# Performance work log

Hardware: AMD Instinct MI355X
Metric: run time of the kernel (lower is better)

## Reference

```python
import jax, jax.numpy as jnp
import numpy as np

N_NODES = 50000
N_EDGES = 800000
NEG_SLOPE = 0.2  # GATConv default
BN_EPS = 1e-5


def _seg_softmax(logits, seg, n):
    # per-target-node softmax over incoming edges (PyG softmax w/ +1e-16)
    m = jax.ops.segment_max(logits, seg, num_segments=n)
    m = jnp.where(jnp.isfinite(m), m, 0.0)
    e = jnp.exp(logits - m[seg])
    s = jax.ops.segment_sum(e, seg, num_segments=n)
    return e / (s[seg] + 1e-16)


def _gat_conv(x, src, dst, W, a_src, a_dst, b, concat):
    # x: [N, Fin]; W: [Fin, H*C]; a_src/a_dst: [H, C]
    n = x.shape[0]
    H, C = a_src.shape
    h = (x @ W).reshape(n, H, C)
    al_s = jnp.einsum('nhc,hc->nh', h, a_src)
    al_d = jnp.einsum('nhc,hc->nh', h, a_dst)
    logits = jax.nn.leaky_relu(al_s[src] + al_d[dst], NEG_SLOPE)  # [E, H]
    alpha = _seg_softmax(logits, dst, n)                           # [E, H]
    out = jax.ops.segment_sum(h[src] * alpha[:, :, None], dst, num_segments=n)
    out = out.reshape(n, H * C) if concat else out.mean(axis=1)
    return out + b


def _bn(x, g, b):
    mu = jnp.mean(x, axis=0)
    var = jnp.mean((x - mu) ** 2, axis=0)
    return (x - mu) * jax.lax.rsqrt(var + BN_EPS) * g + b


def _gat_params(key, fin, heads, ch, scale=0.1):
    k1, k2, k3 = jax.random.split(key, 3)
    W = jax.random.normal(k1, (fin, heads * ch), jnp.float32) * scale
    a_s = jax.random.normal(k2, (heads, ch), jnp.float32) * scale
    a_d = jax.random.normal(k3, (heads, ch), jnp.float32) * scale
    return W, a_s, a_d


def setup_inputs() -> dict:
    key = jax.random.key(0)
    ks = jax.random.split(key, 12)
    inp = {}
    inp['x'] = jax.random.normal(ks[0], (N_NODES, 3), jnp.float32)
    inp['edge_index'] = jax.random.randint(ks[1], (2, N_EDGES), 0, N_NODES, jnp.int64 if jax.config.jax_enable_x64 else jnp.int32)
    inp['W11'], inp['as11'], inp['ad11'] = _gat_params(ks[2], 3, 8, 8)
    inp['b11'] = jnp.zeros((64,), jnp.float32)
    inp['W12'], inp['as12'], inp['ad12'] = _gat_params(ks[3], 64, 8, 8)
    inp['b12'] = jnp.zeros((64,), jnp.float32)
    inp['g1'] = jnp.ones((64,), jnp.float32)
    inp['be1'] = jnp.zeros((64,), jnp.float32)
    inp['W21'], inp['as21'], inp['ad21'] = _gat_params(ks[4], 64, 8, 32)
    inp['b21'] = jnp.zeros((256,), jnp.float32)
    inp['W22'], inp['as22'], inp['ad22'] = _gat_params(ks[5], 256, 8, 32)
    inp['b22'] = jnp.zeros((256,), jnp.float32)
    inp['g2'] = jnp.ones((256,), jnp.float32)
    inp['be2'] = jnp.zeros((256,), jnp.float32)
    inp['W31'], inp['as31'], inp['ad31'] = _gat_params(ks[6], 256, 8, 64)
    inp['b31'] = jnp.zeros((512,), jnp.float32)
    inp['W32'], inp['as32'], inp['ad32'] = _gat_params(ks[7], 512, 8, 1)
    inp['b32'] = jnp.zeros((1,), jnp.float32)
    return inp


def reference(x, edge_index,
              W11, as11, ad11, b11, W12, as12, ad12, b12, g1, be1,
              W21, as21, ad21, b21, W22, as22, ad22, b22, g2, be2,
              W31, as31, ad31, b31, W32, as32, ad32, b32):
    n = x.shape[0]
    loops = jnp.arange(n, dtype=edge_index.dtype)
    src = jnp.concatenate([edge_index[0], loops])  # add_self_loops=True
    dst = jnp.concatenate([edge_index[1], loops])
    # GAT(3, 64, 2): conv -> relu -> conv
    h = jax.nn.relu(_gat_conv(x, src, dst, W11, as11, ad11, b11, True))
    h = _gat_conv(h, src, dst, W12, as12, ad12, b12, True)
    h = jax.nn.leaky_relu(_bn(h, g1, be1), 0.1)
    # GAT(64, 256, 2)
    h = jax.nn.relu(_gat_conv(h, src, dst, W21, as21, ad21, b21, True))
    h = _gat_conv(h, src, dst, W22, as22, ad22, b22, True)
    h = jax.nn.leaky_relu(_bn(h, g2, be2), 0.1)
    # GAT(256, 512, 2, 1): conv -> relu -> conv(concat=False)
    h = jax.nn.relu(_gat_conv(h, src, dst, W31, as31, ad31, b31, True))
    h = _gat_conv(h, src, dst, W32, as32, ad32, b32, False)
    return jax.nn.sigmoid(h)
```

## Files before the change

kernel.cpp:

```cpp
#include <hip/hip_runtime.h>
#include <math.h>

typedef short short8 __attribute__((ext_vector_type(8)));
typedef short short4v __attribute__((ext_vector_type(4)));
typedef float f32x4 __attribute__((ext_vector_type(4)));

__device__ __forceinline__ unsigned short f2bf(float v){
  unsigned u = __builtin_bit_cast(unsigned, v);
  u += 0x7FFFu + ((u >> 16) & 1u);
  return (unsigned short)(u >> 16);
}
__device__ __forceinline__ float bf2f(unsigned short b){
  unsigned u = ((unsigned)b) << 16;
  return __builtin_bit_cast(float, u);
}

__global__ void k_deg(const int* __restrict__ dstv, int* __restrict__ deg, int E){
  int e = blockIdx.x*blockDim.x + threadIdx.x;
  if (e < E) atomicAdd(&deg[dstv[e]], 1);
}

__global__ void k_scan(const int* __restrict__ deg, int* __restrict__ off,
                       int* __restrict__ cursor, int N){
  __shared__ int wpre[16];
  __shared__ int s_tot;
  __shared__ int carry;
  int tid = threadIdx.x;
  int lane = tid & 63, wv = tid >> 6;
  if (tid == 0) carry = 0;
  __syncthreads();
  for (int base = 0; base < N; base += 1024){
    int i = base + tid;
    int v = (i < N) ? deg[i] : 0;
    int incl = v;
    #pragma unroll
    for (int d = 1; d < 64; d <<= 1){
      int t = __shfl_up(incl, d, 64);
      if (lane >= d) incl += t;
    }
    if (lane == 63) wpre[wv] = incl;
    __syncthreads();
    if (tid < 16){
      int x = wpre[tid];
      int ix = x;
      #pragma unroll
      for (int d = 1; d < 16; d <<= 1){
        int t = __shfl_up(ix, d, 16);
        if (tid >= d) ix += t;
      }
      wpre[tid] = ix - x;
      if (tid == 15) s_tot = ix;
    }
    __syncthreads();
    int c = carry;
    int excl = c + wpre[wv] + (incl - v);
    if (i < N){ off[i+1] = excl + v; cursor[i] = excl; }
    __syncthreads();
    if (tid == 0) carry = c + s_tot;
    __syncthreads();
  }
  if (tid == 0) off[0] = 0;
}

__global__ void k_fill(const int* __restrict__ srcv, const int* __restrict__ dstv,
                       int* __restrict__ cursor, int* __restrict__ csr, int E){
  int e = blockIdx.x*blockDim.x + threadIdx.x;
  if (e < E){
    int d = dstv[e];
    int p = atomicAdd(&cursor[d], 1);
    csr[p] = srcv[e];
  }
}

__global__ void k_prepAll(const float* __restrict__ W11, const float* __restrict__ W12,
                          const float* __restrict__ W21, const float* __restrict__ W22,
                          const float* __restrict__ W31,
                          unsigned short* __restrict__ bh, unsigned short* __restrict__ bl){
  int i = blockIdx.x*blockDim.x + threadIdx.x;
  if (i >= 221184) return;
  const float* W; int K, kpsh, off, Nn;
  if (i < 4096)       { W=W11; K=3;   kpsh=6; off=0;     Nn=64;  }
  else if (i < 8192)  { W=W12; K=64;  kpsh=6; off=4096;  Nn=64;  }
  else if (i < 24576) { W=W21; K=64;  kpsh=6; off=8192;  Nn=256; }
  else if (i < 90112) { W=W22; K=256; kpsh=8; off=24576; Nn=256; }
  else                { W=W31; K=256; kpsh=8; off=90112; Nn=512; }
  int j = i - off;
  int Kp = 1 << kpsh;
  int n = j >> kpsh, k = j & (Kp-1);
  float v = (k < K) ? W[(size_t)k*Nn + n] : 0.0f;
  unsigned short h = f2bf(v);
  bh[i] = h;
  bl[i] = f2bf(v - bf2f(h));
}

__global__ void k_bn_stats(const unsigned short* __restrict__ x, float* __restrict__ psum,
                           float* __restrict__ psq, int N, int HC){
  int f = threadIdx.x;
  float s = 0.f, q = 0.f;
  for (int r = blockIdx.x; r < N; r += gridDim.x){
    float v = bf2f(x[(size_t)r*HC + f]);
    s += v; q += v*v;
  }
  psum[blockIdx.x*HC + f] = s;
  psq [blockIdx.x*HC + f] = q;
}

__global__ void k_bn_coef(const float* __restrict__ psum, const float* __restrict__ psq,
                          const float* __restrict__ g, const float* __restrict__ b,
                          float* __restrict__ sc, float* __restrict__ sh,
                          float invN, int HC, int nb){
  int f = threadIdx.x + blockIdx.x*blockDim.x;
  if (f >= HC) return;
  float s = 0.f, q = 0.f;
  for (int r = 0; r < nb; ++r){ s += psum[r*HC+f]; q += psq[r*HC+f]; }
  float mu  = s*invN;
  float var = q*invN - mu*mu;
  float rs  = rsqrtf(var + 1e-5f) * g[f];
  sc[f] = rs;
  sh[f] = b[f] - mu*rs;
}

template<int BN, int AFMT>
__global__ __launch_bounds__((BN==64)?256:512)
void gemm_mfma(const void* __restrict__ Av, const unsigned short* __restrict__ Bh,
               const unsigned short* __restrict__ Bl,
               const float* __restrict__ bnsc, const float* __restrict__ bnsh,
               const float* __restrict__ a_s, const float* __restrict__ a_d,
               unsigned short* __restrict__ Pb, float* __restrict__ Ds,
               float* __restrict__ Dd, int M, int K){
  constexpr int WAVES   = (BN==64) ? 4 : 8;
  constexpr int BLOCK   = WAVES*64;
  constexpr int WAVES_N = BN/64;
  constexpr int WAVES_M = WAVES/WAVES_N;
  constexpr int WM      = 64/WAVES_M;
  constexpr int MF      = WM/16;
  constexpr int CH      = (BN==512)?64 : (BN==256)?32 : 8;
  constexpr int TERMS   = (AFMT==2) ? 2 : 3;
  const int Kp = (K + 63) & ~(int)63;

  __shared__ char lds[(TERMS==3)?16384:8192];

  int tid  = threadIdx.x;
  int lane = tid & 63;
  int wid  = tid >> 6;
  int wn = wid % WAVES_N;
  int wm = wid / WAVES_N;
  int n0w = wn*64;
  int wm0 = wm*WM;
  int m0 = blockIdx.x * 64;

  f32x4 acc[MF][4];
  #pragma unroll
  for (int i = 0; i < MF; ++i)
    #pragma unroll
    for (int j = 0; j < 4; ++j)
      acc[i][j] = (f32x4){0.f,0.f,0.f,0.f};

  constexpr int SITER = 512/BLOCK;

  for (int k0 = 0; k0 < Kp; k0 += 64){
    __syncthreads();
    #pragma unroll
    for (int it = 0; it < SITER; ++it){
      int i = it*BLOCK + tid;
      int row = i >> 3, c8 = i & 7;
      int gm = m0 + row;
      int gk = k0 + c8*8;
      int off = row*128 + ((c8 ^ (row&7))<<4);
      if constexpr (AFMT == 2){
        short8 hv = {0,0,0,0,0,0,0,0};
        if (gm < M) hv = *(const short8*)((const unsigned short*)Av + (size_t)gm*K + gk);
        *(short8*)(lds + off) = hv;
      } else if constexpr (AFMT == 1){
        short8 raw = {0,0,0,0,0,0,0,0};
        if (gm < M) raw = *(const short8*)((const unsigned short*)Av + (size_t)gm*K + gk);
        short8 hi, lo;
        #pragma unroll
        for (int j=0;j<8;++j){
          float u = bf2f((unsigned short)raw[j])*bnsc[gk+j] + bnsh[gk+j];
          u = u > 0.f ? u : 0.1f*u;
          if (gm >= M) u = 0.f;
          unsigned short hb = f2bf(u);
          hi[j] = (short)hb;
          lo[j] = (short)f2bf(u - bf2f(hb));
        }
        *(short8*)(lds + off) = hi;
        *(short8*)(lds + 8192 + off) = lo;
      } else {
        const float* A = (const float*)Av;
        float v[8];
        if (gm < M && gk + 8 <= K){
          const float* ap = A + (size_t)gm*K + gk;
          float4 x0 = *(const float4*)ap;
          float4 x1 = *(const float4*)(ap+4);
          v[0]=x0.x; v[1]=x0.y; v[2]=x0.z; v[3]=x0.w;
          v[4]=x1.x; v[5]=x1.y; v[6]=x1.z; v[7]=x1.w;
        } else {
          #pragma unroll
          for (int j=0;j<8;++j){
            int gkj = gk + j;
            v[j] = (gm < M && gkj < K) ? A[(size_t)gm*K + gkj] : 0.0f;
          }
        }
        short8 hi, lo;
        #pragma unroll
        for (int j=0;j<8;++j){
          unsigned short hb = f2bf(v[j]);
          hi[j] = (short)hb;
          lo[j] = (short)f2bf(v[j] - bf2f(hb));
        }
        *(short8*)(lds + off) = hi;
        *(short8*)(lds + 8192 + off) = lo;
      }
    }
    __syncthreads();
    #pragma unroll
    for (int kk = 0; kk < 2; ++kk){
      short8 bhf[4], blf[4];
      #pragma unroll
      for (int nf = 0; nf < 4; ++nf){
        int ncol = n0w + nf*16 + (lane & 15);
        int kidx = k0 + kk*32 + ((lane>>4)<<3);
        size_t bo = (size_t)ncol*Kp + kidx;
        bhf[nf] = *(const short8*)(Bh + bo);
        blf[nf] = *(const short8*)(Bl + bo);
      }
      #pragma unroll
      for (int mt = 0; mt < MF; ++mt){
        int row = wm0 + mt*16 + (lane & 15);
        int c8 = kk*4 + (lane>>4);
        int off = row*128 + ((c8 ^ (row&7))<<4);
        short8 ah = *(const short8*)(lds + off);
        #pragma unroll
        for (int nf = 0; nf < 4; ++nf){
          acc[mt][nf] = __builtin_amdgcn_mfma_f32_16x16x32_bf16(ah, bhf[nf], acc[mt][nf], 0,0,0);
          acc[mt][nf] = __builtin_amdgcn_mfma_f32_16x16x32_bf16(ah, blf[nf], acc[mt][nf], 0,0,0);
        }
        if constexpr (TERMS == 3){
          short8 al = *(const short8*)(lds + 8192 + off);
          #pragma unroll
          for (int nf = 0; nf < 4; ++nf)
            acc[mt][nf] = __builtin_amdgcn_mfma_f32_16x16x32_bf16(al, bhf[nf], acc[mt][nf], 0,0,0);
        }
      }
    }
  }

  float asv[4], adv[4];
  #pragma unroll
  for (int nf=0; nf<4; ++nf){
    int gcol = n0w + nf*16 + (lane&15);
    asv[nf] = a_s[gcol];
    adv[nf] = a_d[gcol];
  }
  #pragma unroll
  for (int mt = 0; mt < MF; ++mt){
    #pragma unroll
    for (int r = 0; r < 4; ++r){
      int gm = m0 + wm0 + mt*16 + ((lane>>4)<<2) + r;
      bool ok = gm < M;
      #pragma unroll
      for (int nf=0;nf<4;++nf){
        if (ok) Pb[(size_t)gm*BN + n0w + nf*16 + (lane&15)] = f2bf(acc[mt][nf][r]);
      }
      if constexpr (CH == 64){
        float ps = acc[mt][0][r]*asv[0] + acc[mt][1][r]*asv[1]
                 + acc[mt][2][r]*asv[2] + acc[mt][3][r]*asv[3];
        float pd = acc[mt][0][r]*adv[0] + acc[mt][1][r]*adv[1]
                 + acc[mt][2][r]*adv[2] + acc[mt][3][r]*adv[3];
        #pragma unroll
        for (int d2=1; d2<16; d2<<=1){ ps += __shfl_xor(ps,d2,64); pd += __shfl_xor(pd,d2,64); }
        if (ok && (lane&15)==0){
          int head = n0w >> 6;
          Ds[(size_t)gm*8 + head] = ps;
          Dd[(size_t)gm*8 + head] = pd;
        }
      } else if constexpr (CH == 32){
        float ps0 = acc[mt][0][r]*asv[0] + acc[mt][1][r]*asv[1];
        float ps1 = acc[mt][2][r]*asv[2] + acc[mt][3][r]*asv[3];
        float pd0 = acc[mt][0][r]*adv[0] + acc[mt][1][r]*adv[1];
        float pd1 = acc[mt][2][r]*adv[2] + acc[mt][3][r]*adv[3];
        #pragma unroll
        for (int d2=1; d2<16; d2<<=1){
          ps0 += __shfl_xor(ps0,d2,64); ps1 += __shfl_xor(ps1,d2,64);
          pd0 += __shfl_xor(pd0,d2,64); pd1 += __shfl_xor(pd1,d2,64);
        }
        if (ok && (lane&15)==0){
          int head = n0w >> 5;
          Ds[(size_t)gm*8 + head]     = ps0;
          Ds[(size_t)gm*8 + head + 1] = ps1;
          Dd[(size_t)gm*8 + head]     = pd0;
          Dd[(size_t)gm*8 + head + 1] = pd1;
        }
      } else {
        #pragma unroll
        for (int nf=0;nf<4;++nf){
          float ps = acc[mt][nf][r]*asv[nf];
          float pd = acc[mt][nf][r]*adv[nf];
          #pragma unroll
          for (int d2=1; d2<8; d2<<=1){ ps += __shfl_xor(ps,d2,64); pd += __shfl_xor(pd,d2,64); }
          if (ok && (lane&7)==0){
            int head = nf*2 + ((lane>>3)&1);
            Ds[(size_t)gm*8 + head] = ps;
            Dd[(size_t)gm*8 + head] = pd;
          }
        }
      }
    }
  }
}

template<int HC, int ACT>
__global__ __launch_bounds__(256)
void k_agg(const unsigned short* __restrict__ Pb, const float* __restrict__ Ds,
           const float* __restrict__ Dd, const int* __restrict__ off,
           const int* __restrict__ csr, const float* __restrict__ bias,
           unsigned short* __restrict__ outb, int N){
  constexpr int R = HC/64;
  constexpr int UF = (R==1) ? 8 : 4;
  __shared__ float salpha[4][512];
  int lane = threadIdx.x & 63;
  int wid  = threadIdx.x >> 6;
  int n = blockIdx.x*4 + wid;
  if (n >= N) return;
  int o0 = off[n], deg = off[n+1]-o0;
  int myh = lane >> 3;

  float aldn[8];
  {
    const float* dn = Dd + (unsigned)n*8u;
    float4 x0 = *(const float4*)dn;
    float4 x1 = *(const float4*)(dn+4);
    aldn[0]=x0.x; aldn[1]=x0.y; aldn[2]=x0.z; aldn[3]=x0.w;
    aldn[4]=x1.x; aldn[5]=x1.y; aldn[6]=x1.z; aldn[7]=x1.w;
  }

  float acc[R];
  #pragma unroll
  for (int j=0;j<R;++j) acc[j]=0.f;

  if (deg < 64){
    int nE = deg + 1;
    int myidx = (lane < deg) ? csr[o0+lane] : n;
    bool active = (lane < nE);
    float v[8];
    {
      const float* dp = Ds + (unsigned)myidx*8u;
      float4 x0 = *(const float4*)dp;
      float4 x1 = *(const float4*)(dp+4);
      float t[8] = {x0.x,x0.y,x0.z,x0.w,x1.x,x1.y,x1.z,x1.w};
      #pragma unroll
      for (int h=0;h<8;++h){
        float u = t[h] + aldn[h];
        u = u > 0.f ? u : 0.2f*u;
        v[h] = active ? u : -1e30f;
      }
    }
    float m[8];
    #pragma unroll
    for (int h=0;h<8;++h) m[h]=v[h];
    #pragma unroll
    for (int d=1; d<64; d<<=1)
      #pragma unroll
      for (int h=0;h<8;++h) m[h] = fmaxf(m[h], __shfl_xor(m[h], d, 64));
    float sv[8], s[8];
    #pragma unroll
    for (int h=0;h<8;++h){ sv[h] = active ? __expf(v[h]-m[h]) : 0.f; s[h]=sv[h]; }
    #pragma unroll
    for (int d=1; d<64; d<<=1)
      #pragma unroll
      for (int h=0;h<8;++h) s[h] += __shfl_xor(s[h], d, 64);
    if (active){
      #pragma unroll
      for (int h=0;h<8;++h) salpha[wid][lane*8+h] = sv[h] / (s[h] + 1e-16f);
    }
    asm volatile("s_waitcnt lgkmcnt(0)" ::: "memory");

    const unsigned short* Pl = Pb + lane*R;
    float accu[UF][R];
    #pragma unroll
    for (int u=0;u<UF;++u)
      #pragma unroll
      for (int j=0;j<R;++j) accu[u][j] = 0.f;

    int e = 0;
    #pragma unroll 1
    for (; e + UF <= nE; e += UF){
      unsigned bse[UF];
      float av[UF];
      #pragma unroll
      for (int u=0;u<UF;++u){
        int sidx = __shfl(myidx, e+u, 64);
        bse[u] = (unsigned)sidx * (unsigned)HC;
        av[u]  = salpha[wid][(e+u)*8 + myh];
      }
      #pragma unroll
      for (int u=0;u<UF;++u){
        if constexpr (R == 1){
          accu[u][0] += av[u] * bf2f(Pl[bse[u]]);
        } else if constexpr (R == 4){
          short4v w = *(const short4v*)(Pl + bse[u]);
          #pragma unroll
          for (int j=0;j<4;++j) accu[u][j] += av[u] * bf2f((unsigned short)w[j]);
        } else {
          short8 w = *(const short8*)(Pl + bse[u]);
          #pragma unroll
          for (int j=0;j<8;++j) accu[u][j] += av[u] * bf2f((unsigned short)w[j]);
        }
      }
    }
    #pragma unroll 1
    for (; e < nE; ++e){
      int sidx = __shfl(myidx, e, 64);
      unsigned bs = (unsigned)sidx * (unsigned)HC;
      float alpha = salpha[wid][e*8 + myh];
      if constexpr (R == 1){
        accu[0][0] += alpha * bf2f(Pl[bs]);
      } else if constexpr (R == 4){
        short4v w = *(const short4v*)(Pl + bs);
        #pragma unroll
        for (int j=0;j<4;++j) accu[0][j] += alpha * bf2f((unsigned short)w[j]);
      } else {
        short8 w = *(const short8*)(Pl + bs);
        #pragma unroll
        for (int j=0;j<8;++j) accu[0][j] += alpha * bf2f((unsigned short)w[j]);
      }
    }
    #pragma unroll
    for (int j=0;j<R;++j){
      float t0 = 0.f;
      #pragma unroll
      for (int u=0;u<UF;++u) t0 += accu[u][j];
      acc[j] = t0;
    }
  } else {
    float m[8];
    #pragma unroll
    for (int h=0;h<8;++h) m[h] = -1e30f;
    for (int e = lane; e <= deg; e += 64){
      int src = (e < deg) ? csr[o0+e] : n;
      const float* ap = Ds + (size_t)src*8;
      #pragma unroll
      for (int h=0;h<8;++h){
        float u = ap[h] + aldn[h];
        u = u > 0.f ? u : 0.2f*u;
        m[h] = fmaxf(m[h], u);
      }
    }
    #pragma unroll
    for (int d=1; d<64; d<<=1)
      #pragma unroll
      for (int h=0;h<8;++h) m[h] = fmaxf(m[h], __shfl_xor(m[h], d, 64));
    float s[8] = {0,0,0,0,0,0,0,0};
    for (int e = lane; e <= deg; e += 64){
      int src = (e < deg) ? csr[o0+e] : n;
      const float* ap = Ds + (size_t)src*8;
      #pragma unroll
      for (int h=0;h<8;++h){
        float u = ap[h] + aldn[h];
        u = u > 0.f ? u : 0.2f*u;
        s[h] += __expf(u - m[h]);
      }
    }
    #pragma unroll
    for (int d=1; d<64; d<<=1)
      #pragma unroll
      for (int h=0;h<8;++h) s[h] += __shfl_xor(s[h], d, 64);
    float mh = m[myh];
    float rsh = 1.0f/(s[myh] + 1e-16f);
    float adh = aldn[myh];
    for (int e = 0; e <= deg; ++e){
      int src = (e < deg) ? csr[o0+e] : n;
      float u = Ds[(size_t)src*8 + myh] + adh;
      u = u > 0.f ? u : 0.2f*u;
      float alpha = __expf(u - mh) * rsh;
      const unsigned short* hp = Pb + (size_t)src*HC + lane*R;
      if constexpr (R == 1){
        acc[0] += alpha * bf2f(hp[0]);
      } else if constexpr (R == 4){
        short4v w = *(const short4v*)hp;
        #pragma unroll
        for (int j=0;j<4;++j) acc[j] += alpha * bf2f((unsigned short)w[j]);
      } else {
        short8 w = *(const short8*)hp;
        #pragma unroll
        for (int j=0;j<8;++j) acc[j] += alpha * bf2f((unsigned short)w[j]);
      }
    }
  }

  #pragma unroll
  for (int j = 0; j < R; ++j){
    int f = lane*R + j;
    float v = acc[j] + bias[f];
    if (ACT == 1) v = fmaxf(v, 0.0f);
    outb[(size_t)n*HC + f] = f2bf(v);
  }
}

__global__ __launch_bounds__(256)
void gemm8(const unsigned short* __restrict__ Qb, const float* __restrict__ W,
           float* __restrict__ h8, int M){
  int lane = threadIdx.x & 63;
  int gw = (blockIdx.x*blockDim.x + threadIdx.x) >> 6;
  int nw = (gridDim.x*blockDim.x) >> 6;
  float w[8][8];
  const float* wp = W + lane*64;
  #pragma unroll
  for (int j=0;j<8;++j){
    float4 a = *(const float4*)(wp + j*8);
    float4 b = *(const float4*)(wp + j*8 + 4);
    w[j][0]=a.x; w[j][1]=a.y; w[j][2]=a.z; w[j][3]=a.w;
    w[j][4]=b.x; w[j][5]=b.y; w[j][6]=b.z; w[j][7]=b.w;
  }
  for (int n = gw; n < M; n += nw){
    short8 v8 = *(const short8*)(Qb + (size_t)n*512 + lane*8);
    float p[8] = {0,0,0,0,0,0,0,0};
    #pragma unroll
    for (int j=0;j<8;++j){
      float x = bf2f((unsigned short)v8[j]);
      #pragma unroll
      for (int o=0;o<8;++o) p[o] += x * w[j][o];
    }
    #pragma unroll
    for (int d=1; d<64; d<<=1)
      #pragma unroll
      for (int o=0;o<8;++o) p[o] += __shfl_xor(p[o], d, 64);
    if (lane == 0){
      float4 y0 = make_float4(p[0],p[1],p[2],p[3]);
      float4 y1 = make_float4(p[4],p[5],p[6],p[7]);
      *(float4*)(h8 + (size_t)n*8)     = y0;
      *(float4*)(h8 + (size_t)n*8 + 4) = y1;
    }
  }
}

__global__ __launch_bounds__(256)
void k_final(const float* __restrict__ h8, const float* __restrict__ a_s,
             const float* __restrict__ a_d, const int* __restrict__ off,
             const int* __restrict__ csr, const float* __restrict__ b32,
             float* __restrict__ outp, int N){
  int lane = threadIdx.x & 63;
  int wv   = threadIdx.x >> 6;
  int n = blockIdx.x*4 + wv;
  if (n >= N) return;
  int o0 = off[n], deg = off[n+1]-o0;
  float asv[8], adv[8];
  #pragma unroll
  for (int h=0;h<8;++h){ asv[h]=a_s[h]; adv[h]=a_d[h]; }
  float aldn[8];
  {
    const float* hp = h8 + (size_t)n*8;
    float4 x0 = *(const float4*)hp;
    float4 x1 = *(const float4*)(hp+4);
    float hn[8] = {x0.x,x0.y,x0.z,x0.w,x1.x,x1.y,x1.z,x1.w};
    #pragma unroll
    for (int h=0;h<8;++h) aldn[h] = hn[h]*adv[h];
  }

  if (deg < 64){
    int nE = deg + 1;
    int src = (lane < deg) ? csr[o0+lane] : n;
    bool act = (lane < nE);
    float hs[8];
    {
      const float* hp = h8 + (size_t)src*8;
      float4 x0 = *(const float4*)hp;
      float4 x1 = *(const float4*)(hp+4);
      hs[0]=x0.x; hs[1]=x0.y; hs[2]=x0.z; hs[3]=x0.w;
      hs[4]=x1.x; hs[5]=x1.y; hs[6]=x1.z; hs[7]=x1.w;
    }
    float v[8];
    #pragma unroll
    for (int h=0;h<8;++h){
      float u = hs[h]*asv[h] + aldn[h];
      u = u > 0.f ? u : 0.2f*u;
      v[h] = act ? u : -1e30f;
    }
    float m[8];
    #pragma unroll
    for (int h=0;h<8;++h) m[h]=v[h];
    #pragma unroll
    for (int d=1; d<64; d<<=1)
      #pragma unroll
      for (int h=0;h<8;++h) m[h] = fmaxf(m[h], __shfl_xor(m[h], d, 64));
    float s[8], t[8];
    #pragma unroll
    for (int h=0;h<8;++h){
      float e = act ? __expf(v[h]-m[h]) : 0.f;
      s[h]=e; t[h]=e*hs[h];
    }
    #pragma unroll
    for (int d=1; d<64; d<<=1)
      #pragma unroll
      for (int h=0;h<8;++h){
        s[h] += __shfl_xor(s[h], d, 64);
        t[h] += __shfl_xor(t[h], d, 64);
      }
    if (lane == 0){
      float o = 0.f;
      #pragma unroll
      for (int h=0;h<8;++h) o += t[h]/(s[h]+1e-16f);
      o = o*0.125f + b32[0];
      outp[n] = 1.0f/(1.0f + __expf(-o));
    }
  } else if (lane == 0){
    float m[8], s[8], agg[8];
    #pragma unroll
    for (int h=0;h<8;++h){ m[h]=-1e30f; s[h]=0.f; agg[h]=0.f; }
    for (int e = 0; e <= deg; ++e){
      int src = (e < deg) ? csr[o0+e] : n;
      #pragma unroll
      for (int h=0;h<8;++h){
        float u = h8[(size_t)src*8+h]*asv[h] + aldn[h];
        u = u > 0.f ? u : 0.2f*u;
        m[h] = fmaxf(m[h], u);
      }
    }
    for (int e = 0; e <= deg; ++e){
      int src = (e < deg) ? csr[o0+e] : n;
      #pragma unroll
      for (int h=0;h<8;++h){
        float u = h8[(size_t)src*8+h]*asv[h] + aldn[h];
        u = u > 0.f ? u : 0.2f*u;
        float ex = __expf(u - m[h]);
        s[h] += ex;
        agg[h] += ex * h8[(size_t)src*8+h];
      }
    }
    float o = 0.f;
    #pragma unroll
    for (int h=0;h<8;++h) o += agg[h]/(s[h]+1e-16f);
    o = o*0.125f + b32[0];
    outp[n] = 1.0f/(1.0f + __expf(-o));
  }
}

extern "C" void kernel_launch(void* const* d_in, const int* in_sizes, int n_in,
                              void* d_out, int out_size, void* d_ws, size_t ws_size,
                              hipStream_t stream){
  int N = in_sizes[0]/3;
  int E = in_sizes[1]/2;
  const float* x    = (const float*)d_in[0];
  const int*   ei   = (const int*)  d_in[1];
  const float* W11  = (const float*)d_in[2];
  const float* as11 = (const float*)d_in[3];
  const float* ad11 = (const float*)d_in[4];
  const float* b11  = (const float*)d_in[5];
  const float* W12  = (const float*)d_in[6];
  const float* as12 = (const float*)d_in[7];
  const float* ad12 = (const float*)d_in[8];
  const float* b12  = (const float*)d_in[9];
  const float* g1   = (const float*)d_in[10];
  const float* be1  = (const float*)d_in[11];
  const float* W21  = (const float*)d_in[12];
  const float* as21 = (const float*)d_in[13];
  const float* ad21 = (const float*)d_in[14];
  const float* b21  = (const float*)d_in[15];
  const float* W22  = (const float*)d_in[16];
  const float* as22 = (const float*)d_in[17];
  const float* ad22 = (const float*)d_in[18];
  const float* b22  = (const float*)d_in[19];
  const float* g2   = (const float*)d_in[20];
  const float* be2  = (const float*)d_in[21];
  const float* W31  = (const float*)d_in[22];
  const float* as31 = (const float*)d_in[23];
  const float* ad31 = (const float*)d_in[24];
  const float* b31  = (const float*)d_in[25];
  const float* W32  = (const float*)d_in[26];
  const float* as32 = (const float*)d_in[27];
  const float* ad32 = (const float*)d_in[28];
  const float* b32  = (const float*)d_in[29];

  char* ws = (char*)d_ws;
  size_t o = 0;
  auto alloc = [&](size_t bytes)->char*{
    char* p = ws + o;
    o = (o + bytes + 255) & ~(size_t)255;
    return p;
  };
  int*   deg    = (int*)  alloc((size_t)N*4);
  int*   off    = (int*)  alloc((size_t)(N+1)*4);
  int*   cursor = (int*)  alloc((size_t)N*4);
  int*   csr    = (int*)  alloc((size_t)E*4);
  unsigned short* bh = (unsigned short*)alloc(221184*2);
  unsigned short* bl = (unsigned short*)alloc(221184*2);
  float* h8     = (float*)alloc((size_t)N*8*4);
  float* psum   = (float*)alloc(128*256*4);
  float* psq    = (float*)alloc(128*256*4);
  float* bnsc   = (float*)alloc(1024);
  float* bnsh   = (float*)alloc(1024);
  unsigned short* Pb = (unsigned short*)alloc((size_t)N*512*2);
  unsigned short* Qb = (unsigned short*)alloc((size_t)N*512*2);
  float* Dsb    = (float*)alloc((size_t)N*8*4);
  float* Ddb    = (float*)alloc((size_t)N*8*4);
  (void)ws_size;

  const int BT11=0, BT12=4096, BT21=8192, BT22=24576, BT31=90112;

  hipMemsetAsync(deg, 0, (size_t)N*4, stream);
  int eb = (E+255)/256;
  k_deg <<<eb, 256, 0, stream>>>(ei+E, deg, E);
  k_prepAll<<<(221184+255)/256, 256, 0, stream>>>(W11, W12, W21, W22, W31, bh, bl);
  k_scan<<<1, 1024, 0, stream>>>(deg, off, cursor, N);
  k_fill<<<eb, 256, 0, stream>>>(ei, ei+E, cursor, csr, E);

  int mb = (N+63)/64;
  int nb4 = (N+3)/4;
  float invN = 1.0f/(float)N;

  gemm_mfma<64,0><<<mb, 256, 0, stream>>>(x, bh+BT11, bl+BT11, nullptr, nullptr,
                                          as11, ad11, Pb, Dsb, Ddb, N, 3);
  k_agg<64,1><<<nb4, 256, 0, stream>>>(Pb, Dsb, Ddb, off, csr, b11, Qb, N);

  gemm_mfma<64,2><<<mb, 256, 0, stream>>>(Qb, bh+BT12, bl+BT12, nullptr, nullptr,
                                          as12, ad12, Pb, Dsb, Ddb, N, 64);
  k_agg<64,0><<<nb4, 256, 0, stream>>>(Pb, Dsb, Ddb, off, csr, b12, Qb, N);
  k_bn_stats<<<128, 64, 0, stream>>>(Qb, psum, psq, N, 64);
  k_bn_coef<<<1, 64, 0, stream>>>(psum, psq, g1, be1, bnsc, bnsh, invN, 64, 128);

  gemm_mfma<256,1><<<mb, 512, 0, stream>>>(Qb, bh+BT21, bl+BT21, bnsc, bnsh,
                                           as21, ad21, Pb, Dsb, Ddb, N, 64);
  k_agg<256,1><<<nb4, 256, 0, stream>>>(Pb, Dsb, Ddb, off, csr, b21, Qb, N);

  gemm_mfma<256,2><<<mb, 512, 0, stream>>>(Qb, bh+BT22, bl+BT22, nullptr, nullptr,
                                           as22, ad22, Pb, Dsb, Ddb, N, 256);
  k_agg<256,0><<<nb4, 256, 0, stream>>>(Pb, Dsb, Ddb, off, csr, b22, Qb, N);
  k_bn_stats<<<128, 256, 0, stream>>>(Qb, psum, psq, N, 256);
  k_bn_coef<<<1, 256, 0, stream>>>(psum, psq, g2, be2, bnsc, bnsh, invN, 256, 128);

  gemm_mfma<512,1><<<mb, 512, 0, stream>>>(Qb, bh+BT31, bl+BT31, bnsc, bnsh,
                                           as31, ad31, Pb, Dsb, Ddb, N, 256);
  k_agg<512,1><<<nb4, 256, 0, stream>>>(Pb, Dsb, Ddb, off, csr, b31, Qb, N);

  gemm8<<<1024, 256, 0, stream>>>(Qb, W32, h8, N);
  k_final<<<nb4, 256, 0, stream>>>(h8, as32, ad32, off, csr, b32,
                                   (float*)d_out, N);
}
```

Baseline: 1.270 ms.

## Split edges across sub-wave lane groups in aggregation, widen BN stats, fuse prep kernels

The low-degree aggregation path now gives each HC variant its own lane mapping. For HC=64 and HC=256, the wave is split into 4 or 2 sub-groups that process different edges in parallel with vector loads, then combine results with xor shuffles and vector stores. The unrolled multi-accumulator loop is removed. BN statistics now use full 256-thread blocks with more partial slots, and the degree count and weight prep kernels are merged into one launch. This is meant to raise memory-level parallelism in the gather and to cut the serial BN reduction and launch overhead, at the cost of losing the explicit unrolling in the HC=512 path.

```diff
diff --git a/kernel.cpp b/kernel.cpp
--- a/kernel.cpp
+++ b/kernel.cpp
@@ -15,9 +15,28 @@
   return __builtin_bit_cast(float, u);
 }
 
-__global__ void k_deg(const int* __restrict__ dstv, int* __restrict__ deg, int E){
-  int e = blockIdx.x*blockDim.x + threadIdx.x;
-  if (e < E) atomicAdd(&deg[dstv[e]], 1);
+__global__ void k_deg_prep(const int* __restrict__ dstv, int* __restrict__ deg, int E,
+                           const float* __restrict__ W11, const float* __restrict__ W12,
+                           const float* __restrict__ W21, const float* __restrict__ W22,
+                           const float* __restrict__ W31,
+                           unsigned short* __restrict__ bh, unsigned short* __restrict__ bl){
+  int i = blockIdx.x*blockDim.x + threadIdx.x;
+  if (i < E) atomicAdd(&deg[dstv[i]], 1);
+  if (i < 221184){
+    const float* W; int K, kpsh, off, Nn;
+    if (i < 4096)       { W=W11; K=3;   kpsh=6; off=0;     Nn=64;  }
+    else if (i < 8192)  { W=W12; K=64;  kpsh=6; off=4096;  Nn=64;  }
+    else if (i < 24576) { W=W21; K=64;  kpsh=6; off=8192;  Nn=256; }
+    else if (i < 90112) { W=W22; K=256; kpsh=8; off=24576; Nn=256; }
+    else                { W=W31; K=256; kpsh=8; off=90112; Nn=512; }
+    int j = i - off;
+    int Kp = 1 << kpsh;
+    int n = j >> kpsh, k = j & (Kp-1);
+    float v = (k < K) ? W[(size_t)k*Nn + n] : 0.0f;
+    unsigned short h = f2bf(v);
+    bh[i] = h;
+    bl[i] = f2bf(v - bf2f(h));
+  }
 }
 
 __global__ void k_scan(const int* __restrict__ deg, int* __restrict__ off,
@@ -72,37 +91,21 @@
   }
 }
 
-__global__ void k_prepAll(const float* __restrict__ W11, const float* __restrict__ W12,
-                          const float* __restrict__ W21, const float* __restrict__ W22,
-                          const float* __restrict__ W31,
-                          unsigned short* __restrict__ bh, unsigned short* __restrict__ bl){
-  int i = blockIdx.x*blockDim.x + threadIdx.x;
-  if (i >= 221184) return;
-  const float* W; int K, kpsh, off, Nn;
-  if (i < 4096)       { W=W11; K=3;   kpsh=6; off=0;     Nn=64;  }
-  else if (i < 8192)  { W=W12; K=64;  kpsh=6; off=4096;  Nn=64;  }
-  else if (i < 24576) { W=W21; K=64;  kpsh=6; off=8192;  Nn=256; }
-  else if (i < 90112) { W=W22; K=256; kpsh=8; off=24576; Nn=256; }
-  else                { W=W31; K=256; kpsh=8; off=90112; Nn=512; }
-  int j = i - off;
-  int Kp = 1 << kpsh;
-  int n = j >> kpsh, k = j & (Kp-1);
-  float v = (k < K) ? W[(size_t)k*Nn + n] : 0.0f;
-  unsigned short h = f2bf(v);
-  bh[i] = h;
-  bl[i] = f2bf(v - bf2f(h));
-}
-
-__global__ void k_bn_stats(const unsigned short* __restrict__ x, float* __restrict__ psum,
-                           float* __restrict__ psq, int N, int HC){
-  int f = threadIdx.x;
+__global__ __launch_bounds__(256)
+void k_bn_stats(const unsigned short* __restrict__ x, float* __restrict__ psum,
+                float* __restrict__ psq, int N, int HC){
+  int f   = threadIdx.x & (HC-1);
+  int sub = threadIdx.x / HC;
+  int subs = 256 / HC;
+  int slot = blockIdx.x*subs + sub;
+  int stride = gridDim.x*subs;
   float s = 0.f, q = 0.f;
-  for (int r = blockIdx.x; r < N; r += gridDim.x){
+  for (int r = slot; r < N; r += stride){
     float v = bf2f(x[(size_t)r*HC + f]);
     s += v; q += v*v;
   }
-  psum[blockIdx.x*HC + f] = s;
-  psq [blockIdx.x*HC + f] = q;
+  psum[(size_t)slot*HC + f] = s;
+  psq [(size_t)slot*HC + f] = q;
 }
 
 __global__ void k_bn_coef(const float* __restrict__ psum, const float* __restrict__ psq,
@@ -112,7 +115,7 @@
   int f = threadIdx.x + blockIdx.x*blockDim.x;
   if (f >= HC) return;
   float s = 0.f, q = 0.f;
-  for (int r = 0; r < nb; ++r){ s += psum[r*HC+f]; q += psq[r*HC+f]; }
+  for (int r = 0; r < nb; ++r){ s += psum[(size_t)r*HC+f]; q += psq[(size_t)r*HC+f]; }
   float mu  = s*invN;
   float var = q*invN - mu*mu;
   float rs  = rsqrtf(var + 1e-5f) * g[f];
@@ -316,15 +319,12 @@
            const float* __restrict__ Dd, const int* __restrict__ off,
            const int* __restrict__ csr, const float* __restrict__ bias,
            unsigned short* __restrict__ outb, int N){
-  constexpr int R = HC/64;
-  constexpr int UF = (R==1) ? 8 : 4;
   __shared__ float salpha[4][512];
   int lane = threadIdx.x & 63;
   int wid  = threadIdx.x >> 6;
   int n = blockIdx.x*4 + wid;
   if (n >= N) return;
   int o0 = off[n], deg = off[n+1]-o0;
-  int myh = lane >> 3;
 
   float aldn[8];
   {
@@ -334,10 +334,6 @@
     aldn[0]=x0.x; aldn[1]=x0.y; aldn[2]=x0.z; aldn[3]=x0.w;
     aldn[4]=x1.x; aldn[5]=x1.y; aldn[6]=x1.z; aldn[7]=x1.w;
   }
-
-  float acc[R];
-  #pragma unroll
-  for (int j=0;j<R;++j) acc[j]=0.f;
 
   if (deg < 64){
     int nE = deg + 1;
@@ -376,64 +372,85 @@
     }
     asm volatile("s_waitcnt lgkmcnt(0)" ::: "memory");
 
-    const unsigned short* Pl = Pb + lane*R;
-    float accu[UF][R];
-    #pragma unroll
-    for (int u=0;u<UF;++u)
-      #pragma unroll
-      for (int j=0;j<R;++j) accu[u][j] = 0.f;
-
-    int e = 0;
-    #pragma unroll 1
-    for (; e + UF <= nE; e += UF){
-      unsigned bse[UF];
-      float av[UF];
-      #pragma unroll
-      for (int u=0;u<UF;++u){
-        int sidx = __shfl(myidx, e+u, 64);
-        bse[u] = (unsigned)sidx * (unsigned)HC;
-        av[u]  = salpha[wid][(e+u)*8 + myh];
-      }
-      #pragma unroll
-      for (int u=0;u<UF;++u){
-        if constexpr (R == 1){
-          accu[u][0] += av[u] * bf2f(Pl[bse[u]]);
-        } else if constexpr (R == 4){
-          short4v w = *(const short4v*)(Pl + bse[u]);
-          #pragma unroll
-          for (int j=0;j<4;++j) accu[u][j] += av[u] * bf2f((unsigned short)w[j]);
-        } else {
-          short8 w = *(const short8*)(Pl + bse[u]);
-          #pragma unroll
-          for (int j=0;j<8;++j) accu[u][j] += av[u] * bf2f((unsigned short)w[j]);
-        }
-      }
-    }
-    #pragma unroll 1
-    for (; e < nE; ++e){
-      int sidx = __shfl(myidx, e, 64);
-      unsigned bs = (unsigned)sidx * (unsigned)HC;
-      float alpha = salpha[wid][e*8 + myh];
-      if constexpr (R == 1){
-        accu[0][0] += alpha * bf2f(Pl[bs]);
-      } else if constexpr (R == 4){
-        short4v w = *(const short4v*)(Pl + bs);
-        #pragma unroll
-        for (int j=0;j<4;++j) accu[0][j] += alpha * bf2f((unsigned short)w[j]);
-      } else {
-        short8 w = *(const short8*)(Pl + bs);
-        #pragma unroll
-        for (int j=0;j<8;++j) accu[0][j] += alpha * bf2f((unsigned short)w[j]);
-      }
-    }
-    #pragma unroll
-    for (int j=0;j<R;++j){
-      float t0 = 0.f;
-      #pragma unroll
-      for (int u=0;u<UF;++u) t0 += accu[u][j];
-      acc[j] = t0;
+    if constexpr (HC == 512){
+      int myh = lane >> 3;
+      float acc[8] = {0,0,0,0,0,0,0,0};
+      const unsigned short* Pl = Pb + lane*8;
+      for (int e=0; e<nE; ++e){
+        int src = __shfl(myidx, e, 64);
+        float alpha = salpha[wid][e*8 + myh];
+        short8 w = *(const short8*)(Pl + (unsigned)src*512u);
+        #pragma unroll
+        for (int j=0;j<8;++j) acc[j] += alpha * bf2f((unsigned short)w[j]);
+      }
+      #pragma unroll
+      for (int j=0;j<8;++j){
+        int f = lane*8 + j;
+        float u = acc[j] + bias[f];
+        if (ACT == 1) u = fmaxf(u, 0.0f);
+        outb[(unsigned)n*512u + f] = f2bf(u);
+      }
+    } else if constexpr (HC == 256){
+      int sub = lane >> 5, fl = lane & 31;
+      int h = fl >> 2;
+      float acc[8] = {0,0,0,0,0,0,0,0};
+      const unsigned short* Pl = Pb + fl*8;
+      for (int e=0; e<nE; e+=2){
+        int eg = e + sub;
+        bool val = eg < nE;
+        int src = __shfl(myidx, val ? eg : 0, 64);
+        float alpha = val ? salpha[wid][eg*8 + h] : 0.f;
+        short8 w = *(const short8*)(Pl + (unsigned)src*256u);
+        #pragma unroll
+        for (int j=0;j<8;++j) acc[j] += alpha * bf2f((unsigned short)w[j]);
+      }
+      #pragma unroll
+      for (int j=0;j<8;++j) acc[j] += __shfl_xor(acc[j], 32, 64);
+      if (sub == 0){
+        short8 ov;
+        #pragma unroll
+        for (int j=0;j<8;++j){
+          int f = fl*8 + j;
+          float u = acc[j] + bias[f];
+          if (ACT == 1) u = fmaxf(u, 0.0f);
+          ov[j] = (short)f2bf(u);
+        }
+        *(short8*)(outb + (unsigned)n*256u + fl*8) = ov;
+      }
+    } else {
+      int sub = lane >> 4, fl = lane & 15;
+      int h = fl >> 1;
+      float acc[4] = {0,0,0,0};
+      const unsigned short* Pl = Pb + fl*4;
+      for (int e=0; e<nE; e+=4){
+        int eg = e + sub;
+        bool val = eg < nE;
+        int src = __shfl(myidx, val ? eg : 0, 64);
+        float alpha = val ? salpha[wid][eg*8 + h] : 0.f;
+        short4v w = *(const short4v*)(Pl + (unsigned)src*64u);
+        #pragma unroll
+        for (int j=0;j<4;++j) acc[j] += alpha * bf2f((unsigned short)w[j]);
+      }
+      #pragma unroll
+      for (int j=0;j<4;++j){
+        acc[j] += __shfl_xor(acc[j], 16, 64);
+        acc[j] += __shfl_xor(acc[j], 32, 64);
+      }
+      if (sub == 0){
+        short4v ov;
+        #pragma unroll
+        for (int j=0;j<4;++j){
+          int f = fl*4 + j;
+          float u = acc[j] + bias[f];
+          if (ACT == 1) u = fmaxf(u, 0.0f);
+          ov[j] = (short)f2bf(u);
+        }
+        *(short4v*)(outb + (unsigned)n*64u + fl*4) = ov;
+      }
     }
   } else {
+    constexpr int R = HC/64;
+    int myh = lane >> 3;
     float m[8];
     #pragma unroll
     for (int h=0;h<8;++h) m[h] = -1e30f;
@@ -469,6 +486,9 @@
     float mh = m[myh];
     float rsh = 1.0f/(s[myh] + 1e-16f);
     float adh = aldn[myh];
+    float acc[R];
+    #pragma unroll
+    for (int j=0;j<R;++j) acc[j]=0.f;
     for (int e = 0; e <= deg; ++e){
       int src = (e < deg) ? csr[o0+e] : n;
       float u = Ds[(size_t)src*8 + myh] + adh;
@@ -487,14 +507,13 @@
         for (int j=0;j<8;++j) acc[j] += alpha * bf2f((unsigned short)w[j]);
       }
     }
-  }
-
-  #pragma unroll
-  for (int j = 0; j < R; ++j){
-    int f = lane*R + j;
-    float v = acc[j] + bias[f];
-    if (ACT == 1) v = fmaxf(v, 0.0f);
-    outb[(size_t)n*HC + f] = f2bf(v);
+    #pragma unroll
+    for (int j = 0; j < R; ++j){
+      int f = lane*R + j;
+      float u = acc[j] + bias[f];
+      if (ACT == 1) u = fmaxf(u, 0.0f);
+      outb[(size_t)n*HC + f] = f2bf(u);
+    }
   }
 }
 
@@ -686,8 +705,8 @@
   unsigned short* bh = (unsigned short*)alloc(221184*2);
   unsigned short* bl = (unsigned short*)alloc(221184*2);
   float* h8     = (float*)alloc((size_t)N*8*4);
-  float* psum   = (float*)alloc(128*256*4);
-  float* psq    = (float*)alloc(128*256*4);
+  float* psum   = (float*)alloc(1024*64*4);
+  float* psq    = (float*)alloc(1024*64*4);
   float* bnsc   = (float*)alloc(1024);
   float* bnsh   = (float*)alloc(1024);
   unsigned short* Pb = (unsigned short*)alloc((size_t)N*512*2);
@@ -700,8 +719,7 @@
 
   hipMemsetAsync(deg, 0, (size_t)N*4, stream);
   int eb = (E+255)/256;
-  k_deg <<<eb, 256, 0, stream>>>(ei+E, deg, E);
-  k_prepAll<<<(221184+255)/256, 256, 0, stream>>>(W11, W12, W21, W22, W31, bh, bl);
+  k_deg_prep<<<eb, 256, 0, stream>>>(ei+E, deg, E, W11, W12, W21, W22, W31, bh, bl);
   k_scan<<<1, 1024, 0, stream>>>(deg, off, cursor, N);
   k_fill<<<eb, 256, 0, stream>>>(ei, ei+E, cursor, csr, E);
 
@@ -716,8 +734,8 @@
   gemm_mfma<64,2><<<mb, 256, 0, stream>>>(Qb, bh+BT12, bl+BT12, nullptr, nullptr,
                                           as12, ad12, Pb, Dsb, Ddb, N, 64);
   k_agg<64,0><<<nb4, 256, 0, stream>>>(Pb, Dsb, Ddb, off, csr, b12, Qb, N);
-  k_bn_stats<<<128, 64, 0, stream>>>(Qb, psum, psq, N, 64);
-  k_bn_coef<<<1, 64, 0, stream>>>(psum, psq, g1, be1, bnsc, bnsh, invN, 64, 128);
+  k_bn_stats<<<256, 256, 0, stream>>>(Qb, psum, psq, N, 64);
+  k_bn_coef<<<1, 64, 0, stream>>>(psum, psq, g1, be1, bnsc, bnsh, invN, 64, 1024);
 
   gemm_mfma<256,1><<<mb, 512, 0, stream>>>(Qb, bh+BT21, bl+BT21, bnsc, bnsh,
                                            as21, ad21, Pb, Dsb, Ddb, N, 64);
@@ -726,8 +744,8 @@
   gemm_mfma<256,2><<<mb, 512, 0, stream>>>(Qb, bh+BT22, bl+BT22, nullptr, nullptr,
                                            as22, ad22, Pb, Dsb, Ddb, N, 256);
   k_agg<256,0><<<nb4, 256, 0, stream>>>(Pb, Dsb, Ddb, off, csr, b22, Qb, N);
-  k_bn_stats<<<128, 256, 0, stream>>>(Qb, psum, psq, N, 256);
-  k_bn_coef<<<1, 256, 0, stream>>>(psum, psq, g2, be2, bnsc, bnsh, invN, 256, 128);
+  k_bn_stats<<<256, 256, 0, stream>>>(Qb, psum, psq, N, 256);
+  k_bn_coef<<<1, 256, 0, stream>>>(psum, psq, g2, be2, bnsc, bnsh, invN, 256, 256);
 
   gemm_mfma<512,1><<<mb, 512, 0, stream>>>(Qb, bh+BT31, bl+BT31, bnsc, bnsh,
                                            as31, ad31, Pb, Dsb, Ddb, N, 256);
```

After: 1.376 ms. 1.08x slower.
